# Kernel tuning notes

Hardware: AMD Instinct MI355X
Metric: run time of the kernel (lower is better)

Reference implementation:

```python
import jax, jax.numpy as jnp
import numpy as np

N_NODES, N_EDGES, N_GRAPHS = 100000, 400000, 4096
F_NODE, F_EDGE, G = 78, 11, 256
NUM_LAYERS, NUM_TIMESTEPS = 3, 2
L = NUM_LAYERS - 1  # number of GNNLayers after GetContext


def _lrelu(x):
    return jax.nn.leaky_relu(x, 0.01)


def _seg_softmax(logits, seg, n):
    # softmax of logits grouped by segment id (edge_softmax over dst / softmax_nodes over graph)
    m = jax.ops.segment_max(logits, seg, num_segments=n)
    e = jnp.exp(logits - m[seg])
    s = jax.ops.segment_sum(e, seg, num_segments=n)
    return e / s[seg]


def _gru(x, h, Wih, Whh, bih, bhh):
    gi = x @ Wih.T + bih
    gh = h @ Whh.T + bhh
    ir, iz, inn = jnp.split(gi, 3, axis=-1)
    hr, hz, hn = jnp.split(gh, 3, axis=-1)
    r = jax.nn.sigmoid(ir + hr)
    z = jax.nn.sigmoid(iz + hz)
    nn_ = jnp.tanh(inn + r * hn)
    return (1.0 - z) * nn_ + z * h


def _forward(node_feats, edge_feats, W_pn, b_pn, W_pe1, b_pe1, W_pe2, b_pe2, W_et, b_et,
             gru0_Wih, gru0_Whh, gru0_bih, gru0_bhh,
             gnn_W_pe, gnn_b_pe, gnn_W_pn, gnn_b_pn, gnn_Wih, gnn_Whh, gnn_bih, gnn_bhh,
             ro_W_cl, ro_b_cl, ro_W_pn, ro_b_pn, ro_Wih, ro_Whh, ro_bih, ro_bhh,
             ln_gamma, ln_beta, src, dst, node_graph):
    N, B = node_feats.shape[0], N_GRAPHS
    # ---- GetContext ----
    hv_new = _lrelu(node_feats @ W_pn.T + b_pn)                                  # [N,G]
    he1 = _lrelu(jnp.concatenate([node_feats[src], edge_feats], -1) @ W_pe1.T + b_pe1)  # [E,G]
    logits = _lrelu(jnp.concatenate([hv_new[dst], he1], -1) @ W_pe2.T + b_pe2)   # [E,1]
    a = _seg_softmax(logits, dst, N)
    c = jax.ops.segment_sum(a * (he1 @ W_et.T + b_et), dst, num_segments=N)      # [N,G]
    h = jax.nn.relu(_gru(jax.nn.elu(c), hv_new, gru0_Wih, gru0_Whh, gru0_bih, gru0_bhh))
    # ---- GNNLayers (AttentiveGRU2) ----
    for l in range(L):
        lg = _lrelu(jnp.concatenate([h[dst], h[src]], -1) @ gnn_W_pe[l].T + gnn_b_pe[l])  # [E,1]
        a = _seg_softmax(lg, dst, N)
        hv = h @ gnn_W_pn[l].T + gnn_b_pn[l]
        c = jax.ops.segment_sum(a * hv[src], dst, num_segments=N)
        h = jax.nn.relu(_gru(jax.nn.elu(c), h, gnn_Wih[l], gnn_Whh[l], gnn_bih[l], gnn_bhh[l]))
    # ---- AttentiveFPReadout ----
    g_feats = jax.ops.segment_sum(h, node_graph, num_segments=B)                 # [B,G]
    for t in range(NUM_TIMESTEPS):
        z = _lrelu(jnp.concatenate([jax.nn.relu(g_feats)[node_graph], h], -1) @ ro_W_cl[t].T + ro_b_cl[t])  # [N,1]
        a = _seg_softmax(z, node_graph, B)
        hv = h @ ro_W_pn[t].T + ro_b_pn[t]
        gr = jax.ops.segment_sum(a * hv, node_graph, num_segments=B)
        g_feats = jax.nn.relu(_gru(jax.nn.elu(gr), g_feats, ro_Wih[t], ro_Whh[t], ro_bih[t], ro_bhh[t]))
    # ---- LayerNorm (dropout is identity at inference) ----
    mu = jnp.mean(g_feats, -1, keepdims=True)
    var = jnp.mean((g_feats - mu) ** 2, -1, keepdims=True)
    return (g_feats - mu) / jnp.sqrt(var + 1e-5) * ln_gamma + ln_beta


def setup_inputs() -> dict:
    key = jax.random.key(0)
    ks = iter(jax.random.split(key, 64))

    def nrm(shape, scale=1.0):
        return jax.random.normal(next(ks), shape, dtype=jnp.float32) * scale

    def lin(out_d, in_d):
        return nrm((out_d, in_d), 1.0 / np.sqrt(in_d))

    d = {}
    d['node_feats'] = nrm((N_NODES, F_NODE))
    d['edge_feats'] = nrm((N_EDGES, F_EDGE))
    d['src'] = jax.random.randint(next(ks), (N_EDGES,), 0, N_NODES)
    d['dst'] = jax.random.randint(next(ks), (N_EDGES,), 0, N_NODES)
    d['node_graph'] = jnp.sort(jax.random.randint(next(ks), (N_NODES,), 0, N_GRAPHS))
    # GetContext params
    d['W_pn'] = lin(G, F_NODE); d['b_pn'] = jnp.zeros((G,), jnp.float32)
    d['W_pe1'] = lin(G, F_NODE + F_EDGE); d['b_pe1'] = jnp.zeros((G,), jnp.float32)
    d['W_pe2'] = lin(1, 2 * G); d['b_pe2'] = jnp.zeros((1,), jnp.float32)
    d['W_et'] = lin(G, G); d['b_et'] = jnp.zeros((G,), jnp.float32)
    d['gru0_Wih'] = lin(3 * G, G); d['gru0_Whh'] = lin(3 * G, G)
    d['gru0_bih'] = jnp.zeros((3 * G,), jnp.float32); d['gru0_bhh'] = jnp.zeros((3 * G,), jnp.float32)
    # stacked GNNLayer params
    s2g = 1.0 / np.sqrt(2 * G); sg = 1.0 / np.sqrt(G)
    d['gnn_W_pe'] = nrm((L, 1, 2 * G), s2g); d['gnn_b_pe'] = jnp.zeros((L, 1), jnp.float32)
    d['gnn_W_pn'] = nrm((L, G, G), sg); d['gnn_b_pn'] = jnp.zeros((L, G), jnp.float32)
    d['gnn_Wih'] = nrm((L, 3 * G, G), sg); d['gnn_Whh'] = nrm((L, 3 * G, G), sg)
    d['gnn_bih'] = jnp.zeros((L, 3 * G), jnp.float32); d['gnn_bhh'] = jnp.zeros((L, 3 * G), jnp.float32)
    # stacked readout (GlobalPool) params
    T = NUM_TIMESTEPS
    d['ro_W_cl'] = nrm((T, 1, 2 * G), s2g); d['ro_b_cl'] = jnp.zeros((T, 1), jnp.float32)
    d['ro_W_pn'] = nrm((T, G, G), sg); d['ro_b_pn'] = jnp.zeros((T, G), jnp.float32)
    d['ro_Wih'] = nrm((T, 3 * G, G), sg); d['ro_Whh'] = nrm((T, 3 * G, G), sg)
    d['ro_bih'] = jnp.zeros((T, 3 * G), jnp.float32); d['ro_bhh'] = jnp.zeros((T, 3 * G), jnp.float32)
    d['ln_gamma'] = jnp.ones((G,), jnp.float32); d['ln_beta'] = jnp.zeros((G,), jnp.float32)
    return d


def reference(node_feats, edge_feats, src, dst, node_graph, W_pn, b_pn, W_pe1, b_pe1, W_pe2, b_pe2,
              W_et, b_et, gru0_Wih, gru0_Whh, gru0_bih, gru0_bhh,
              gnn_W_pe, gnn_b_pe, gnn_W_pn, gnn_b_pn, gnn_Wih, gnn_Whh, gnn_bih, gnn_bhh,
              ro_W_cl, ro_b_cl, ro_W_pn, ro_b_pn, ro_Wih, ro_Whh, ro_bih, ro_bhh, ln_gamma, ln_beta):
    return _forward(node_feats, edge_feats, W_pn, b_pn, W_pe1, b_pe1, W_pe2, b_pe2, W_et, b_et,
                    gru0_Wih, gru0_Whh, gru0_bih, gru0_bhh,
                    gnn_W_pe, gnn_b_pe, gnn_W_pn, gnn_b_pn, gnn_Wih, gnn_Whh, gnn_bih, gnn_bhh,
                    ro_W_cl, ro_b_cl, ro_W_pn, ro_b_pn, ro_Wih, ro_Whh, ro_bih, ro_bhh,
                    ln_gamma, ln_beta, src, dst, node_graph)
```

## Files before the change

### kernel.cpp

```cpp
#include <hip/hip_runtime.h>

#define NN 100000
#define NE 400000
#define NB 4096
#define FN 78
#define FE 11
#define GD 256
#define NL 2
#define NT 2

typedef unsigned short u16;
typedef __attribute__((ext_vector_type(8))) short bf16x8;
typedef __attribute__((ext_vector_type(4))) float f32x4;

__device__ __forceinline__ float lrelu_(float x){ return x > 0.f ? x : 0.01f*x; }
__device__ __forceinline__ float elu_(float x){ return x > 0.f ? x : expf(x) - 1.f; }
__device__ __forceinline__ float sigm_(float x){ return 1.f/(1.f + expf(-x)); }

__device__ __forceinline__ float bf2f(u16 u){ return __uint_as_float(((unsigned)u) << 16); }
__device__ __forceinline__ u16 f2bf(float f){
  unsigned u = __float_as_uint(f);
  unsigned r = (u + 0x7fffu + ((u >> 16) & 1u)) >> 16;
  return (u16)r;
}

__global__ void k_zero(float* p, size_t n){
  size_t i = (size_t)blockIdx.x*blockDim.x + threadIdx.x;
  size_t st = (size_t)gridDim.x*blockDim.x;
  for (; i < n; i += st) p[i] = 0.f;
}

__global__ void k_count(const int* __restrict__ dst, int* __restrict__ cnt, int E){
  int e = blockIdx.x*256 + threadIdx.x;
  if (e < E) atomicAdd(&cnt[dst[e]], 1);
}
__global__ void k_scan1(const int* __restrict__ cnt, int* __restrict__ part,
                        int* __restrict__ btot, int n){
  __shared__ int sd[256];
  int i = blockIdx.x*256 + threadIdx.x;
  int v = (i < n) ? cnt[i] : 0;
  sd[threadIdx.x] = v; __syncthreads();
  for (int d=1; d<256; d<<=1){
    int t = (threadIdx.x >= d) ? sd[threadIdx.x-d] : 0;
    __syncthreads();
    sd[threadIdx.x] += t;
    __syncthreads();
  }
  if (i < n) part[i] = sd[threadIdx.x];
  if (threadIdx.x == 255) btot[blockIdx.x] = sd[255];
}
__global__ void k_scan2(const int* __restrict__ btot, int* __restrict__ boff, int nb){
  __shared__ int sd[512];
  int tid = threadIdx.x;
  int v = (tid < nb) ? btot[tid] : 0;
  sd[tid] = v; __syncthreads();
  for (int d=1; d<512; d<<=1){
    int t = (tid >= d) ? sd[tid-d] : 0;
    __syncthreads();
    sd[tid] += t;
    __syncthreads();
  }
  if (tid < nb) boff[tid] = sd[tid] - v;
}
__global__ void k_scan3(const int* __restrict__ part, const int* __restrict__ boff,
                        int* __restrict__ rowptr, int n){
  int i = blockIdx.x*256 + threadIdx.x;
  if (i < n) rowptr[i+1] = part[i] + boff[blockIdx.x];
  if (i == 0) rowptr[0] = 0;
}
__global__ void k_cursor(const int* __restrict__ rowptr, int* __restrict__ cursor, int n){
  int i = blockIdx.x*256 + threadIdx.x;
  if (i < n) cursor[i] = rowptr[i];
}
__global__ void k_fill(const int* __restrict__ dst, int* __restrict__ cursor,
                       int* __restrict__ order, int E){
  int e = blockIdx.x*256 + threadIdx.x;
  if (e < E){
    int pos = atomicAdd(&cursor[dst[e]], 1);
    order[pos] = e;
  }
}
__global__ void k_gpb(const int* __restrict__ ng, int* __restrict__ gpb, int N, int B){
  int b = blockIdx.x*256 + threadIdx.x;
  if (b > B) return;
  int lo = 0, hi = N;
  while (lo < hi){ int mid = (lo+hi)>>1; if (ng[mid] < b) lo = mid+1; else hi = mid; }
  gpb[b] = lo;
}

__global__ void k_pack_b(const float* __restrict__ W, u16* __restrict__ Bp, int OUT, int K){
  int t = blockIdx.x*256 + threadIdx.x;
  if (t >= OUT*K) return;
  int j = t & 7;
  int l = (t >> 3) & 63;
  int rest = t >> 9;
  int nks = K >> 5;
  int ks = rest % nks, c = rest / nks;
  int col = c*16 + (l & 15);
  int k = ks*32 + (l >> 4)*8 + j;
  Bp[t] = f2bf(W[(size_t)col*K + k]);
}

__global__ void k_pack_rz(const float* __restrict__ Wih, const float* __restrict__ Whh,
                          u16* __restrict__ Bp){
  int t = blockIdx.x*256 + threadIdx.x;
  int j = t & 7;
  int l = (t >> 3) & 63;
  int rest = t >> 9;
  int ks = rest & 15, c = rest >> 4;
  int srcrow = (c & 1)*256 + (c >> 1)*16 + (l & 15);
  int k = ks*32 + (l >> 4)*8 + j;
  float v = (k < 256) ? Wih[(size_t)srcrow*GD + k] : Whh[(size_t)srcrow*GD + (k - 256)];
  Bp[t] = f2bf(v);
}

template<int TN>
__global__ void k_node_proj(const float* __restrict__ nf, const float* __restrict__ W, int ldw,
                            const float* __restrict__ b, int act, u16* __restrict__ outb, int N){
  __shared__ float sx[TN][FN];
  int base = blockIdx.x*TN, tid = threadIdx.x;
  for (int i = tid; i < TN*FN; i += 256){
    int n = i / FN, k = i % FN;
    int row = base + n;
    sx[n][k] = (row < N) ? nf[(size_t)row*FN + k] : 0.f;
  }
  __syncthreads();
  int j = tid;
  float acc[TN];
  #pragma unroll
  for (int n=0;n<TN;n++) acc[n]=0.f;
  for (int k=0;k<FN;k++){
    float w = W[(size_t)j*ldw + k];
    #pragma unroll
    for (int n=0;n<TN;n++) acc[n] += w*sx[n][k];
  }
  float bb = b ? b[j] : 0.f;
  #pragma unroll
  for (int n=0;n<TN;n++){
    int row = base + n;
    if (row < N){
      float v = acc[n] + bb;
      outb[(size_t)row*GD + j] = f2bf(act ? lrelu_(v) : v);
    }
  }
}

__global__ void k_dot2_bf16(const u16* __restrict__ rows, const float* __restrict__ wv,
                            float* __restrict__ za, float* __restrict__ zb, int N){
  int wav = threadIdx.x >> 6, lane = threadIdx.x & 63;
  int i = blockIdx.x*4 + wav;
  if (i >= N) return;
  int c0 = lane*4;
  ushort4 r4 = *(const ushort4*)&rows[(size_t)i*GD + c0];
  float4 wa = *(const float4*)&wv[c0];
  float4 wb = *(const float4*)&wv[GD + c0];
  float v0 = bf2f(r4.x), v1 = bf2f(r4.y), v2 = bf2f(r4.z), v3 = bf2f(r4.w);
  float va = v0*wa.x + v1*wa.y + v2*wa.z + v3*wa.w;
  float vb = v0*wb.x + v1*wb.y + v2*wb.z + v3*wb.w;
  #pragma unroll
  for (int off=32; off; off>>=1){ va += __shfl_down(va, off); vb += __shfl_down(vb, off); }
  if (lane == 0){ za[i] = va; zb[i] = vb; }
}

__global__ void k_dot1_bf16(const u16* __restrict__ rows, const float* __restrict__ wv,
                            float* __restrict__ z, int N){
  int wav = threadIdx.x >> 6, lane = threadIdx.x & 63;
  int i = blockIdx.x*4 + wav;
  if (i >= N) return;
  int c0 = lane*4;
  ushort4 r4 = *(const ushort4*)&rows[(size_t)i*GD + c0];
  float4 wa = *(const float4*)&wv[c0];
  float va = bf2f(r4.x)*wa.x + bf2f(r4.y)*wa.y + bf2f(r4.z)*wa.z + bf2f(r4.w)*wa.w;
  #pragma unroll
  for (int off=32; off; off>>=1) va += __shfl_down(va, off);
  if (lane == 0) z[i] = va;
}

__global__ void k_dotg_relu(const float* __restrict__ g, const float* __restrict__ wv,
                            float* __restrict__ zg, int B){
  int wav = threadIdx.x >> 6, lane = threadIdx.x & 63;
  int i = blockIdx.x*4 + wav;
  if (i >= B) return;
  int c0 = lane*4;
  float4 gv = *(const float4*)&g[(size_t)i*GD + c0];
  float4 wa = *(const float4*)&wv[c0];
  float va = fmaxf(gv.x,0.f)*wa.x + fmaxf(gv.y,0.f)*wa.y + fmaxf(gv.z,0.f)*wa.z + fmaxf(gv.w,0.f)*wa.w;
  #pragma unroll
  for (int off=32; off; off>>=1) va += __shfl_down(va, off);
  if (lane == 0) zg[i] = va;
}

__global__ void __launch_bounds__(256)
k_ctx_fused(const u16* __restrict__ P, const float* __restrict__ za,
            const int* __restrict__ order, const int* __restrict__ rowptr,
            const int* __restrict__ src, const float* __restrict__ ef,
            const float* __restrict__ Wpe1, const float* __restrict__ bpe1,
            const float* __restrict__ Wpe2, const float* __restrict__ bpe2,
            u16* __restrict__ wc, float* __restrict__ sdeg, int N){
  int wv = threadIdx.x >> 6, lane = threadIdx.x & 63;
  int d = blockIdx.x*4 + wv;
  if (d >= N) return;
  int j0 = rowptr[d], j1 = rowptr[d+1];
  int c0 = lane*4;
  float wb0 = Wpe2[GD+c0], wb1 = Wpe2[GD+c0+1], wb2 = Wpe2[GD+c0+2], wb3 = Wpe2[GD+c0+3];
  float bp0 = bpe1[c0], bp1 = bpe1[c0+1], bp2 = bpe1[c0+2], bp3 = bpe1[c0+3];
  float wk0[FE], wk1[FE], wk2[FE], wk3[FE];
  #pragma unroll
  for (int k=0;k<FE;k++){
    wk0[k] = Wpe1[(size_t)(c0+0)*(FN+FE) + FN + k];
    wk1[k] = Wpe1[(size_t)(c0+1)*(FN+FE) + FN + k];
    wk2[k] = Wpe1[(size_t)(c0+2)*(FN+FE) + FN + k];
    wk3[k] = Wpe1[(size_t)(c0+3)*(FN+FE) + FN + k];
  }
  float zad = za[d] + bpe2[0];
  float m = -1e30f, s = 0.f;
  float a0=0.f, a1=0.f, a2=0.f, a3=0.f;
  for (int j=j0; j<j1; j++){
    int e = order[j];
    int sn = src[e];
    ushort4 p4 = *(const ushort4*)&P[(size_t)sn*GD + c0];
    const float* efp = &ef[(size_t)e*FE];
    float efv[FE];
    #pragma unroll
    for (int k=0;k<FE;k++) efv[k] = efp[k];
    float h0 = bf2f(p4.x)+bp0, h1 = bf2f(p4.y)+bp1, h2 = bf2f(p4.z)+bp2, h3 = bf2f(p4.w)+bp3;
    #pragma unroll
    for (int k=0;k<FE;k++){
      h0 += wk0[k]*efv[k]; h1 += wk1[k]*efv[k]; h2 += wk2[k]*efv[k]; h3 += wk3[k]*efv[k];
    }
    h0 = lrelu_(h0); h1 = lrelu_(h1); h2 = lrelu_(h2); h3 = lrelu_(h3);
    float part = h0*wb0 + h1*wb1 + h2*wb2 + h3*wb3;
    #pragma unroll
    for (int off=32; off; off>>=1) part += __shfl_down(part, off);
    float l = lrelu_(part + zad);
    l = __shfl(l, 0);
    float mn = fmaxf(m, l);
    float sc = __expf(m - mn);
    float p  = __expf(l - mn);
    s = s*sc + p;
    a0 = a0*sc + p*h0; a1 = a1*sc + p*h1; a2 = a2*sc + p*h2; a3 = a3*sc + p*h3;
    m = mn;
  }
  float inv = (j1 > j0) ? 1.f/s : 0.f;
  ushort4 o;
  o.x = f2bf(a0*inv); o.y = f2bf(a1*inv); o.z = f2bf(a2*inv); o.w = f2bf(a3*inv);
  *(ushort4*)&wc[(size_t)d*GD + c0] = o;
  if (lane == 0) sdeg[d] = (j1 > j0) ? 1.f : 0.f;
}

__global__ void __launch_bounds__(256)
k_gnn_fused(const u16* __restrict__ hv, const float* __restrict__ za, const float* __restrict__ zb,
            const int* __restrict__ order, const int* __restrict__ rowptr,
            const int* __restrict__ src, const float* __restrict__ bias,
            u16* __restrict__ cw, int N){
  int wv = threadIdx.x >> 6, lane = threadIdx.x & 63;
  int d = blockIdx.x*4 + wv;
  if (d >= N) return;
  int j0 = rowptr[d], j1 = rowptr[d+1];
  int c0 = lane*4;
  float zad = za[d] + bias[0];
  float m = -1e30f, s = 0.f;
  float a0=0.f, a1=0.f, a2=0.f, a3=0.f;
  for (int j=j0; j<j1; j++){
    int e = order[j];
    int sn = src[e];
    float l = lrelu_(zad + zb[sn]);
    ushort4 r4 = *(const ushort4*)&hv[(size_t)sn*GD + c0];
    float mn = fmaxf(m, l);
    float sc = __expf(m - mn);
    float p  = __expf(l - mn);
    s = s*sc + p;
    a0 = a0*sc + p*bf2f(r4.x);
    a1 = a1*sc + p*bf2f(r4.y);
    a2 = a2*sc + p*bf2f(r4.z);
    a3 = a3*sc + p*bf2f(r4.w);
    m = mn;
  }
  float inv = (j1 > j0) ? 1.f/s : 0.f;
  ushort4 o;
  o.x = f2bf(elu_(a0*inv)); o.y = f2bf(elu_(a1*inv));
  o.z = f2bf(elu_(a2*inv)); o.w = f2bf(elu_(a3*inv));
  *(ushort4*)&cw[(size_t)d*GD + c0] = o;
}

__global__ void __launch_bounds__(256)
k_ro_fused(const u16* __restrict__ hv, const float* __restrict__ zg, const float* __restrict__ zh,
           const int* __restrict__ gpb, const float* __restrict__ bias,
           float* __restrict__ gr, int B){
  int b = blockIdx.x, tid = threadIdx.x;
  int i0 = gpb[b], i1 = gpb[b+1];
  float zgb = zg[b] + bias[0];
  __shared__ float red[256];
  float lm = -1e30f;
  for (int i = i0 + tid; i < i1; i += 256) lm = fmaxf(lm, lrelu_(zgb + zh[i]));
  red[tid] = lm; __syncthreads();
  for (int d2=128; d2; d2>>=1){ if (tid < d2) red[tid] = fmaxf(red[tid], red[tid+d2]); __syncthreads(); }
  float M = red[0]; __syncthreads();
  float ls = 0.f;
  for (int i = i0 + tid; i < i1; i += 256) ls += __expf(lrelu_(zgb + zh[i]) - M);
  red[tid] = ls; __syncthreads();
  for (int d2=128; d2; d2>>=1){ if (tid < d2) red[tid] += red[tid+d2]; __syncthreads(); }
  float S = red[0];
  float acc = 0.f;
  for (int i = i0; i < i1; i++){
    float p = __expf(lrelu_(zgb + zh[i]) - M);
    acc += p * bf2f(hv[(size_t)i*GD + tid]);
  }
  gr[(size_t)b*GD + tid] = (i1 > i0) ? acc/S : 0.f;
}

__global__ void k_segsum_sorted(const u16* __restrict__ h, const int* __restrict__ gpb,
                                float* __restrict__ g, int B){
  int b = blockIdx.x, tid = threadIdx.x;
  int i0 = gpb[b], i1 = gpb[b+1];
  float acc = 0.f;
  for (int i = i0; i < i1; i++) acc += bf2f(h[(size_t)i*GD + tid]);
  g[(size_t)b*GD + tid] = acc;
}

__global__ void __launch_bounds__(512)
k_gru_mfma32(const u16* __restrict__ x, const u16* __restrict__ hprev,
             const u16* __restrict__ rzp, const u16* __restrict__ nip, const u16* __restrict__ nhp,
             const float* __restrict__ bih, const float* __restrict__ bhh,
             u16* __restrict__ hout, int R){
  int tid = threadIdx.x;
  int wv = tid >> 6, lane = tid & 63;
  int m = lane & 15, kg = lane >> 4;
  int r0 = blockIdx.x*32;

  f32x4 arz[2][4], ani[2][2], anh[2][2];
  #pragma unroll
  for (int rt=0;rt<2;rt++){
    #pragma unroll
    for (int t=0;t<4;t++) arz[rt][t] = (f32x4)(0.f);
    #pragma unroll
    for (int t=0;t<2;t++){ ani[rt][t] = (f32x4)(0.f); anh[rt][t] = (f32x4)(0.f); }
  }

  #pragma unroll
  for (int ks=0; ks<8; ks++){
    int koff = ks*32 + kg*8;
    bf16x8 ax[2], ah[2];
    #pragma unroll
    for (int rt=0; rt<2; rt++){
      int row = r0 + rt*16 + m;
      ax[rt] = *(const bf16x8*)&x[(size_t)row*GD + koff];
      ah[rt] = *(const bf16x8*)&hprev[(size_t)row*GD + koff];
    }
    #pragma unroll
    for (int t=0;t<4;t++){
      int c = wv*4 + t;
      bf16x8 bx = *(const bf16x8*)&rzp[(size_t)((c*16 + ks    )*64 + lane)*8];
      bf16x8 bh = *(const bf16x8*)&rzp[(size_t)((c*16 + ks + 8)*64 + lane)*8];
      #pragma unroll
      for (int rt=0; rt<2; rt++){
        arz[rt][t] = __builtin_amdgcn_mfma_f32_16x16x32_bf16(ax[rt], bx, arz[rt][t], 0, 0, 0);
        arz[rt][t] = __builtin_amdgcn_mfma_f32_16x16x32_bf16(ah[rt], bh, arz[rt][t], 0, 0, 0);
      }
    }
    #pragma unroll
    for (int t=0;t<2;t++){
      int c = wv*2 + t;
      bf16x8 bi = *(const bf16x8*)&nip[(size_t)((c*8 + ks)*64 + lane)*8];
      bf16x8 bh = *(const bf16x8*)&nhp[(size_t)((c*8 + ks)*64 + lane)*8];
      #pragma unroll
      for (int rt=0; rt<2; rt++){
        ani[rt][t] = __builtin_amdgcn_mfma_f32_16x16x32_bf16(ax[rt], bi, ani[rt][t], 0, 0, 0);
        anh[rt][t] = __builtin_amdgcn_mfma_f32_16x16x32_bf16(ah[rt], bh, anh[rt][t], 0, 0, 0);
      }
    }
  }

  #pragma unroll
  for (int g=0; g<2; g++){
    int ch = (wv*2 + g)*16 + m;
    float brz_r = bih[ch] + bhh[ch];
    float brz_z = bih[ch+GD] + bhh[ch+GD];
    float bin   = bih[ch+2*GD];
    float bhn   = bhh[ch+2*GD];
    #pragma unroll
    for (int rt=0; rt<2; rt++){
      #pragma unroll
      for (int i=0;i<4;i++){
        int row = r0 + rt*16 + kg*4 + i;
        float rr = sigm_(arz[rt][2*g  ][i] + brz_r);
        float zz = sigm_(arz[rt][2*g+1][i] + brz_z);
        float nn = tanhf(ani[rt][g][i] + bin + rr*(anh[rt][g][i] + bhn));
        float hp = bf2f(hprev[(size_t)row*GD + ch]);
        float o = (1.f - zz)*nn + zz*hp;
        hout[(size_t)row*GD + ch] = f2bf(fmaxf(o, 0.f));
      }
    }
  }
}

template<int DO_ELU>
__global__ void __launch_bounds__(512)
k_proj_mfma64(const u16* __restrict__ X, const u16* __restrict__ Wp,
              const float* __restrict__ b, u16* __restrict__ Y, int R,
              const float* __restrict__ mask){
  int tid = threadIdx.x;
  int wv = tid >> 6, lane = tid & 63;
  int m = lane & 15, kg = lane >> 4;
  int r0 = blockIdx.x*64;
  f32x4 acc[2][4];
  #pragma unroll
  for (int t=0;t<2;t++)
    #pragma unroll
    for (int rt=0;rt<4;rt++) acc[t][rt] = (f32x4)(0.f);
  #pragma unroll
  for (int ks=0; ks<8; ks++){
    int koff = ks*32 + kg*8;
    bf16x8 a[4];
    #pragma unroll
    for (int rt=0; rt<4; rt++){
      int row = r0 + rt*16 + m;
      if (row > R-1) row = R-1;
      a[rt] = *(const bf16x8*)&X[(size_t)row*GD + koff];
    }
    #pragma unroll
    for (int t=0;t<2;t++){
      int c = wv*2 + t;
      bf16x8 bv = *(const bf16x8*)&Wp[(size_t)((c*8 + ks)*64 + lane)*8];
      #pragma unroll
      for (int rt=0; rt<4; rt++)
        acc[t][rt] = __builtin_amdgcn_mfma_f32_16x16x32_bf16(a[rt], bv, acc[t][rt], 0, 0, 0);
    }
  }
  #pragma unroll
  for (int t=0;t<2;t++){
    int col = wv*32 + t*16 + m;
    float bb = b[col];
    #pragma unroll
    for (int rt=0; rt<4; rt++){
      #pragma unroll
      for (int i=0;i<4;i++){
        int row = r0 + rt*16 + kg*4 + i;
        if (row < R){
          float v = acc[t][rt][i] + bb;
          if (DO_ELU){
            float mk = (mask[row] > 0.f) ? 1.f : 0.f;
            v = elu_(v*mk);
          }
          Y[(size_t)row*GD + col] = f2bf(v);
        }
      }
    }
  }
}

__global__ void __launch_bounds__(256)
k_gru_mfma_f32(const float* __restrict__ x, const float* __restrict__ hprev,
               const u16* __restrict__ Wihp, const u16* __restrict__ Whhp,
               const float* __restrict__ bih, const float* __restrict__ bhh,
               float* __restrict__ hout, int R){
  int tid = threadIdx.x;
  int wave = tid >> 6, lane = tid & 63;
  int m = lane & 15, kg = lane >> 4;
  int r0 = blockIdx.x*16;

  f32x4 agi[3][4], agh[3][4];
  #pragma unroll
  for (int g=0;g<3;g++)
    #pragma unroll
    for (int t=0;t<4;t++){ agi[g][t] = (f32x4)(0.f); agh[g][t] = (f32x4)(0.f); }

  #pragma unroll
  for (int ks=0; ks<8; ks++){
    int koff = ks*32 + kg*8;
    const float* xp = x + (size_t)(r0 + m)*GD + koff;
    float4 x0 = *(const float4*)xp;
    float4 x1 = *(const float4*)(xp+4);
    bf16x8 ax;
    ax[0]=(short)f2bf(elu_(x0.x)); ax[1]=(short)f2bf(elu_(x0.y));
    ax[2]=(short)f2bf(elu_(x0.z)); ax[3]=(short)f2bf(elu_(x0.w));
    ax[4]=(short)f2bf(elu_(x1.x)); ax[5]=(short)f2bf(elu_(x1.y));
    ax[6]=(short)f2bf(elu_(x1.z)); ax[7]=(short)f2bf(elu_(x1.w));
    const float* hr = hprev + (size_t)(r0 + m)*GD + koff;
    float4 h0 = *(const float4*)hr;
    float4 h1 = *(const float4*)(hr+4);
    bf16x8 ah;
    ah[0]=(short)f2bf(h0.x); ah[1]=(short)f2bf(h0.y); ah[2]=(short)f2bf(h0.z); ah[3]=(short)f2bf(h0.w);
    ah[4]=(short)f2bf(h1.x); ah[5]=(short)f2bf(h1.y); ah[6]=(short)f2bf(h1.z); ah[7]=(short)f2bf(h1.w);
    #pragma unroll
    for (int g=0;g<3;g++){
      #pragma unroll
      for (int t=0;t<4;t++){
        int c = g*16 + wave*4 + t;
        bf16x8 bi = *(const bf16x8*)&Wihp[(size_t)((c*8 + ks)*64 + lane)*8];
        bf16x8 bh = *(const bf16x8*)&Whhp[(size_t)((c*8 + ks)*64 + lane)*8];
        agi[g][t] = __builtin_amdgcn_mfma_f32_16x16x32_bf16(ax, bi, agi[g][t], 0, 0, 0);
        agh[g][t] = __builtin_amdgcn_mfma_f32_16x16x32_bf16(ah, bh, agh[g][t], 0, 0, 0);
      }
    }
  }
  #pragma unroll
  for (int t=0;t<4;t++){
    int col = wave*64 + t*16 + m;
    float bir = bih[col],      bhr = bhh[col];
    float biz = bih[col+GD],   bhz = bhh[col+GD];
    float bin = bih[col+2*GD], bhn = bhh[col+2*GD];
    #pragma unroll
    for (int i=0;i<4;i++){
      int row = r0 + kg*4 + i;
      float rr = sigm_(agi[0][t][i] + bir + agh[0][t][i] + bhr);
      float zz = sigm_(agi[1][t][i] + biz + agh[1][t][i] + bhz);
      float nn = tanhf(agi[2][t][i] + bin + rr*(agh[2][t][i] + bhn));
      float hp = hprev[(size_t)row*GD + col];
      float o = (1.f - zz)*nn + zz*hp;
      hout[(size_t)row*GD + col] = fmaxf(o, 0.f);
    }
  }
}

__global__ void k_layernorm(const float* __restrict__ gb, const float* __restrict__ gamma,
                            const float* __restrict__ beta, float* __restrict__ outb){
  int r = blockIdx.x, j = threadIdx.x;
  float v = gb[(size_t)r*GD + j];
  float s1 = v, s2 = v*v;
  #pragma unroll
  for (int off=32; off; off>>=1){ s1 += __shfl_down(s1, off); s2 += __shfl_down(s2, off); }
  __shared__ float r1[4], r2[4];
  int wv = j >> 6, lane = j & 63;
  if (lane == 0){ r1[wv] = s1; r2[wv] = s2; }
  __syncthreads();
  float S1 = r1[0]+r1[1]+r1[2]+r1[3];
  float S2 = r2[0]+r2[1]+r2[2]+r2[3];
  float mu = S1/(float)GD;
  float var = fmaxf(S2/(float)GD - mu*mu, 0.f);
  outb[(size_t)r*GD + j] = (v - mu)/sqrtf(var + 1e-5f)*gamma[j] + beta[j];
}

extern "C" void kernel_launch(void* const* d_in, const int* in_sizes, int n_in,
                              void* d_out, int out_size, void* d_ws, size_t ws_size,
                              hipStream_t stream){
  const float* node_feats = (const float*)d_in[0];
  const float* edge_feats = (const float*)d_in[1];
  const int*   src        = (const int*)d_in[2];
  const int*   dst        = (const int*)d_in[3];
  const int*   node_graph = (const int*)d_in[4];
  const float* W_pn   = (const float*)d_in[5];
  const float* b_pn   = (const float*)d_in[6];
  const float* W_pe1  = (const float*)d_in[7];
  const float* b_pe1  = (const float*)d_in[8];
  const float* W_pe2  = (const float*)d_in[9];
  const float* b_pe2  = (const float*)d_in[10];
  const float* W_et   = (const float*)d_in[11];
  const float* b_et   = (const float*)d_in[12];
  const float* g0_Wih = (const float*)d_in[13];
  const float* g0_Whh = (const float*)d_in[14];
  const float* g0_bih = (const float*)d_in[15];
  const float* g0_bhh = (const float*)d_in[16];
  const float* gnn_W_pe = (const float*)d_in[17];
  const float* gnn_b_pe = (const float*)d_in[18];
  const float* gnn_W_pn = (const float*)d_in[19];
  const float* gnn_b_pn = (const float*)d_in[20];
  const float* gnn_Wih  = (const float*)d_in[21];
  const float* gnn_Whh  = (const float*)d_in[22];
  const float* gnn_bih  = (const float*)d_in[23];
  const float* gnn_bhh  = (const float*)d_in[24];
  const float* ro_W_cl = (const float*)d_in[25];
  const float* ro_b_cl = (const float*)d_in[26];
  const float* ro_W_pn = (const float*)d_in[27];
  const float* ro_b_pn = (const float*)d_in[28];
  const float* ro_Wih  = (const float*)d_in[29];
  const float* ro_Whh  = (const float*)d_in[30];
  const float* ro_bih  = (const float*)d_in[31];
  const float* ro_bhh  = (const float*)d_in[32];
  const float* ln_gamma = (const float*)d_in[33];
  const float* ln_beta  = (const float*)d_in[34];
  float* outp = (float*)d_out;

  const int NBLK = (NN + 255)/256;

  char* w = (char*)d_ws;
  size_t need = 0;
  float* gbuf  = (float*)(w + need); need += (size_t)NB*GD*4;
  float* grbuf = (float*)(w + need); need += (size_t)NB*GD*4;
  float* za    = (float*)(w + need); need += (size_t)NN*4;
  float* zb    = (float*)(w + need); need += (size_t)NN*4;
  float* zg    = (float*)(w + need); need += (size_t)NB*4;
  float* sdeg  = (float*)(w + need); need += (size_t)NN*4;
  int*   cnt    = (int*)(w + need); need += (size_t)NN*4;
  int*   rowptr = (int*)(w + need); need += (size_t)(NN+1)*4;
  int*   cursor = (int*)(w + need); need += (size_t)NN*4;
  int*   order  = (int*)(w + need); need += (size_t)NE*4;
  int*   gpb    = (int*)(w + need); need += (size_t)(NB+1)*4;
  int*   btot   = (int*)(w + need); need += (size_t)512*4;
  int*   boff   = (int*)(w + need); need += (size_t)512*4;
  u16*   hbuf = (u16*)(w + need); need += (size_t)NN*GD*2;
  u16*   htmp = (u16*)(w + need); need += (size_t)NN*GD*2;
  u16*   cwb  = (u16*)(w + need); need += (size_t)NN*GD*2;
  u16*   dbuf = (u16*)(w + need); need += (size_t)NN*GD*2;
  u16* pGruN = (u16*)(w + need); need += (size_t)3*393216*2;
  u16* pGruR = (u16*)(w + need); need += (size_t)4*196608*2;
  u16* pPn  = (u16*)(w + need); need += (size_t)4*GD*GD*2;
  u16* pEt  = (u16*)(w + need); need += (size_t)GD*GD*2;
  if (ws_size < need) return;
  u16* Pbuf   = hbuf;
  u16* hv_new = htmp;

  const size_t LW = 393216;
  const size_t OW = 196608;
  const size_t PW = (size_t)GD*GD;
  const int G64 = (NN + 63)/64;
  const int G32 = NN/32;

  k_zero<<<64, 256, 0, stream>>>((float*)cnt, (size_t)NN);
  k_count<<<(NE+255)/256, 256, 0, stream>>>(dst, cnt, NE);
  k_scan1<<<NBLK, 256, 0, stream>>>(cnt, cnt, btot, NN);
  k_scan2<<<1, 512, 0, stream>>>(btot, boff, NBLK);
  k_scan3<<<NBLK, 256, 0, stream>>>(cnt, boff, rowptr, NN);
  k_cursor<<<NBLK, 256, 0, stream>>>(rowptr, cursor, NN);
  k_fill<<<(NE+255)/256, 256, 0, stream>>>(dst, cursor, order, NE);
  k_gpb<<<(NB+256)/256, 256, 0, stream>>>(node_graph, gpb, NN, NB);

  const float* wihs[3] = { g0_Wih, gnn_Wih, gnn_Wih + (size_t)3*GD*GD };
  const float* whhs[3] = { g0_Whh, gnn_Whh, gnn_Whh + (size_t)3*GD*GD };
  for (int l=0;l<3;l++){
    k_pack_rz<<<1024, 256, 0, stream>>>(wihs[l], whhs[l], pGruN + l*LW);
    k_pack_b<<<256, 256, 0, stream>>>(wihs[l] + (size_t)512*GD, pGruN + l*LW + 262144, 256, GD);
    k_pack_b<<<256, 256, 0, stream>>>(whhs[l] + (size_t)512*GD, pGruN + l*LW + 327680, 256, GD);
  }
  for (int t=0;t<NT;t++){
    k_pack_b<<<768, 256, 0, stream>>>(ro_Wih + (size_t)t*3*GD*GD, pGruR + (2*t)*OW, 768, GD);
    k_pack_b<<<768, 256, 0, stream>>>(ro_Whh + (size_t)t*3*GD*GD, pGruR + (2*t+1)*OW, 768, GD);
  }
  for (int l=0;l<NL;l++)
    k_pack_b<<<256, 256, 0, stream>>>(gnn_W_pn + (size_t)l*GD*GD, pPn + l*PW, GD, GD);
  for (int t=0;t<NT;t++)
    k_pack_b<<<256, 256, 0, stream>>>(ro_W_pn + (size_t)t*GD*GD, pPn + (2+t)*PW, GD, GD);
  k_pack_b<<<256, 256, 0, stream>>>(W_et, pEt, GD, GD);

  k_node_proj<8><<<(NN+7)/8, 256, 0, stream>>>(node_feats, W_pn, FN, b_pn, 1, hv_new, NN);
  k_node_proj<8><<<(NN+7)/8, 256, 0, stream>>>(node_feats, W_pe1, FN+FE, nullptr, 0, Pbuf, NN);
  k_dot1_bf16<<<(NN+3)/4, 256, 0, stream>>>(hv_new, W_pe2, za, NN);
  k_ctx_fused<<<(NN+3)/4, 256, 0, stream>>>(Pbuf, za, order, rowptr, src, edge_feats,
                                            W_pe1, b_pe1, W_pe2, b_pe2, cwb, sdeg, NN);
  k_proj_mfma64<1><<<G64, 512, 0, stream>>>(cwb, pEt, b_et, dbuf, NN, sdeg);
  k_gru_mfma32<<<G32, 512, 0, stream>>>(dbuf, hv_new, pGruN + 0*LW, pGruN + 0*LW + 262144,
                                        pGruN + 0*LW + 327680, g0_bih, g0_bhh, hbuf, NN);

  for (int l=0; l<NL; l++){
    k_dot2_bf16<<<(NN+3)/4, 256, 0, stream>>>(hbuf, gnn_W_pe + (size_t)l*2*GD, za, zb, NN);
    k_proj_mfma64<0><<<G64, 512, 0, stream>>>(hbuf, pPn + l*PW, gnn_b_pn + (size_t)l*GD,
                                              htmp, NN, nullptr);
    k_gnn_fused<<<(NN+3)/4, 256, 0, stream>>>(htmp, za, zb, order, rowptr, src,
                                              gnn_b_pe + l, cwb, NN);
    k_gru_mfma32<<<G32, 512, 0, stream>>>(cwb, hbuf,
                                pGruN + (1+l)*LW, pGruN + (1+l)*LW + 262144, pGruN + (1+l)*LW + 327680,
                                gnn_bih + (size_t)l*3*GD, gnn_bhh + (size_t)l*3*GD, hbuf, NN);
  }

  k_segsum_sorted<<<NB, 256, 0, stream>>>(hbuf, gpb, gbuf, NB);
  for (int t=0; t<NT; t++){
    k_dotg_relu<<<(NB+3)/4, 256, 0, stream>>>(gbuf, ro_W_cl + (size_t)t*2*GD, zg, NB);
    k_dot1_bf16<<<(NN+3)/4, 256, 0, stream>>>(hbuf, ro_W_cl + (size_t)t*2*GD + GD, za, NN);
    k_proj_mfma64<0><<<G64, 512, 0, stream>>>(hbuf, pPn + (2+t)*PW, ro_b_pn + (size_t)t*GD,
                                              htmp, NN, nullptr);
    k_ro_fused<<<NB, 256, 0, stream>>>(htmp, zg, za, gpb, ro_b_cl + t, grbuf, NB);
    k_gru_mfma_f32<<<NB/16, 256, 0, stream>>>(grbuf, gbuf,
                                pGruR + (2*t)*OW, pGruR + (2*t+1)*OW,
                                ro_bih + (size_t)t*3*GD, ro_bhh + (size_t)t*3*GD, gbuf, NB);
  }
  k_layernorm<<<NB, 256, 0, stream>>>(gbuf, ln_gamma, ln_beta, outp);
}
```

Baseline: 2.179 ms.

## Prefetch next edge in context kernel, two-pass softmax in GNN aggregation, scalarize wave index

The GetContext edge-attention kernel now software-prefetches the next edge's source projection row and edge features while it computes the current edge, hiding gather latency. The GNN aggregation kernel replaces the online softmax with a two-pass scheme: it first finds the segment max, then accumulates without rescaling. This cuts exp calls and serial dependencies, at the cost of a second pass over the indices and scores. The MFMA kernels mark the wave index as wave-uniform via readfirstlane so the compiler can keep it in scalar registers.

Measured after the change: 2.244 ms. 3.0% more time.

```diff
diff --git a/kernel.cpp b/kernel.cpp
--- a/kernel.cpp
+++ b/kernel.cpp
@@ -215,18 +215,33 @@
   float zad = za[d] + bpe2[0];
   float m = -1e30f, s = 0.f;
   float a0=0.f, a1=0.f, a2=0.f, a3=0.f;
+  ushort4 p4c = make_ushort4(0,0,0,0);
+  float efc[FE];
+  #pragma unroll
+  for (int k=0;k<FE;k++) efc[k] = 0.f;
+  if (j0 < j1){
+    int e0 = order[j0];
+    p4c = *(const ushort4*)&P[(size_t)src[e0]*GD + c0];
+    const float* efp = &ef[(size_t)e0*FE];
+    #pragma unroll
+    for (int k=0;k<FE;k++) efc[k] = efp[k];
+  }
   for (int j=j0; j<j1; j++){
-    int e = order[j];
-    int sn = src[e];
-    ushort4 p4 = *(const ushort4*)&P[(size_t)sn*GD + c0];
-    const float* efp = &ef[(size_t)e*FE];
-    float efv[FE];
-    #pragma unroll
-    for (int k=0;k<FE;k++) efv[k] = efp[k];
-    float h0 = bf2f(p4.x)+bp0, h1 = bf2f(p4.y)+bp1, h2 = bf2f(p4.z)+bp2, h3 = bf2f(p4.w)+bp3;
+    ushort4 p4n = p4c;
+    float efn[FE];
+    #pragma unroll
+    for (int k=0;k<FE;k++) efn[k] = 0.f;
+    if (j+1 < j1){
+      int en = order[j+1];
+      p4n = *(const ushort4*)&P[(size_t)src[en]*GD + c0];
+      const float* efp = &ef[(size_t)en*FE];
+      #pragma unroll
+      for (int k=0;k<FE;k++) efn[k] = efp[k];
+    }
+    float h0 = bf2f(p4c.x)+bp0, h1 = bf2f(p4c.y)+bp1, h2 = bf2f(p4c.z)+bp2, h3 = bf2f(p4c.w)+bp3;
     #pragma unroll
     for (int k=0;k<FE;k++){
-      h0 += wk0[k]*efv[k]; h1 += wk1[k]*efv[k]; h2 += wk2[k]*efv[k]; h3 += wk3[k]*efv[k];
+      h0 += wk0[k]*efc[k]; h1 += wk1[k]*efc[k]; h2 += wk2[k]*efc[k]; h3 += wk3[k]*efc[k];
     }
     h0 = lrelu_(h0); h1 = lrelu_(h1); h2 = lrelu_(h2); h3 = lrelu_(h3);
     float part = h0*wb0 + h1*wb1 + h2*wb2 + h3*wb3;
@@ -240,6 +255,9 @@
     s = s*sc + p;
     a0 = a0*sc + p*h0; a1 = a1*sc + p*h1; a2 = a2*sc + p*h2; a3 = a3*sc + p*h3;
     m = mn;
+    p4c = p4n;
+    #pragma unroll
+    for (int k=0;k<FE;k++) efc[k] = efn[k];
   }
   float inv = (j1 > j0) ? 1.f/s : 0.f;
   ushort4 o;
@@ -259,22 +277,23 @@
   int j0 = rowptr[d], j1 = rowptr[d+1];
   int c0 = lane*4;
   float zad = za[d] + bias[0];
-  float m = -1e30f, s = 0.f;
+  float M = -1e30f;
+  for (int j=j0; j<j1; j++){
+    int sn = src[order[j]];
+    M = fmaxf(M, lrelu_(zad + zb[sn]));
+  }
+  float s = 0.f;
   float a0=0.f, a1=0.f, a2=0.f, a3=0.f;
   for (int j=j0; j<j1; j++){
     int e = order[j];
     int sn = src[e];
-    float l = lrelu_(zad + zb[sn]);
+    float p = __expf(lrelu_(zad + zb[sn]) - M);
     ushort4 r4 = *(const ushort4*)&hv[(size_t)sn*GD + c0];
-    float mn = fmaxf(m, l);
-    float sc = __expf(m - mn);
-    float p  = __expf(l - mn);
-    s = s*sc + p;
-    a0 = a0*sc + p*bf2f(r4.x);
-    a1 = a1*sc + p*bf2f(r4.y);
-    a2 = a2*sc + p*bf2f(r4.z);
-    a3 = a3*sc + p*bf2f(r4.w);
-    m = mn;
+    s += p;
+    a0 += p*bf2f(r4.x);
+    a1 += p*bf2f(r4.y);
+    a2 += p*bf2f(r4.z);
+    a3 += p*bf2f(r4.w);
   }
   float inv = (j1 > j0) ? 1.f/s : 0.f;
   ushort4 o;
@@ -324,7 +343,8 @@
              const float* __restrict__ bih, const float* __restrict__ bhh,
              u16* __restrict__ hout, int R){
   int tid = threadIdx.x;
-  int wv = tid >> 6, lane = tid & 63;
+  int wv = __builtin_amdgcn_readfirstlane(tid >> 6);
+  int lane = tid & 63;
   int m = lane & 15, kg = lane >> 4;
   int r0 = blockIdx.x*32;
 
@@ -400,7 +420,8 @@
               const float* __restrict__ b, u16* __restrict__ Y, int R,
               const float* __restrict__ mask){
   int tid = threadIdx.x;
-  int wv = tid >> 6, lane = tid & 63;
+  int wv = __builtin_amdgcn_readfirstlane(tid >> 6);
+  int lane = tid & 63;
   int m = lane & 15, kg = lane >> 4;
   int r0 = blockIdx.x*64;
   f32x4 acc[2][4];
@@ -455,7 +476,8 @@
                const float* __restrict__ bih, const float* __restrict__ bhh,
                float* __restrict__ hout, int R){
   int tid = threadIdx.x;
-  int wave = tid >> 6, lane = tid & 63;
+  int wave = __builtin_amdgcn_readfirstlane(tid >> 6);
+  int lane = tid & 63;
   int m = lane & 15, kg = lane >> 4;
   int r0 = blockIdx.x*16;
 
```
